# Performance work log

Measured on AMD Instinct MI355X. Metric: run time of the kernel, lower is better.

Reference implementation:

```python
import jax, jax.numpy as jnp
import numpy as np

A_NUM = 9
C_NUM = 20


def generate_anchor(anc, grid):
    # anc: (A,2) w,h ; grid: (B,H,W,2) centers -> anchors (B,A,H,W,4)
    centers = grid[:, None]                      # (B,1,H,W,2)
    half = anc.reshape(1, -1, 1, 1, 2) * 0.5     # (1,A,1,1,2)
    return jnp.concatenate([centers - half, centers + half], axis=-1)


def iou_matrix(proposals, bboxes):
    # proposals: (B,A,H,W,4) -> (B,K,4); bboxes: (B,N,5)
    B = proposals.shape[0]
    p = proposals.reshape(B, -1, 4)[:, :, None, :]   # (B,K,1,4)
    bb = bboxes[:, None, :, :]                       # (B,1,N,5)
    s_p = (p[..., 2] - p[..., 0]) * (p[..., 3] - p[..., 1])
    s_b = (bb[..., 2] - bb[..., 0]) * (bb[..., 3] - bb[..., 1])
    ix1 = jnp.maximum(p[..., 0], bb[..., 0])
    iy1 = jnp.maximum(p[..., 1], bb[..., 1])
    ix2 = jnp.minimum(p[..., 2], bb[..., 2])
    iy2 = jnp.minimum(p[..., 3], bb[..., 3])
    s_i = jnp.clip(ix2 - ix1, 0.0) * jnp.clip(iy2 - iy1, 0.0)
    s_u = s_p + s_b - s_i
    iou = jnp.clip(s_i / (s_u + 1e-8), 0.0)
    invalid = (s_u <= 0) | (s_p <= 0) | (s_b <= 0) | (bb[..., 0] < 0)
    return jnp.where(invalid, 0.0, iou)              # (B,K,N)


def extract_anchor_data(anchor_data, idx):
    # anchor_data: (B,A,D,H,W) -> flat (B*A*H*W, D) -> gather
    B, A, D, H, W = anchor_data.shape
    flat = jnp.transpose(anchor_data, (0, 1, 3, 4, 2)).reshape(-1, D)
    return flat[idx]


def extract_class_scores(all_scores, idx, num_anchors):
    # all_scores: (B,C,H,W) -> (B,A,H,W,C) flat -> gather
    B, C, H, W = all_scores.shape
    s = jnp.transpose(all_scores, (0, 2, 3, 1))[:, None]          # (B,1,H,W,C)
    s = jnp.broadcast_to(s, (B, num_anchors, H, W, C)).reshape(-1, C)
    return s[idx]


def setup_inputs() -> dict:
    key = jax.random.key(0)
    ks = jax.random.split(key, 8)
    B, Cin, H, W = 32, 1280, 28, 28
    N, M = 64, 4096
    hid, out_ch = 128, 5 * A_NUM + C_NUM
    features = jax.random.normal(ks[0], (B, Cin, H, W), dtype=jnp.float32)
    # grid of feature-cell centers (GenerateGrid-style)
    xs = jnp.arange(W, dtype=jnp.float32) + 0.5
    ys = jnp.arange(H, dtype=jnp.float32) + 0.5
    gx, gy = jnp.meshgrid(xs, ys, indexing='xy')
    grid = jnp.broadcast_to(jnp.stack([gx, gy], axis=-1), (B, H, W, 2))
    anc = jnp.array([[1.0, 1], [2, 2], [3, 3], [4, 4], [5, 5], [2, 3], [3, 2], [3, 5], [5, 3]], dtype=jnp.float32)
    tl = jax.random.uniform(ks[1], (B, N, 2), minval=0.0, maxval=20.0)
    wh = jax.random.uniform(ks[2], (B, N, 2), minval=1.0, maxval=8.0)
    cls = jax.random.randint(ks[3], (B, N, 1), 0, C_NUM).astype(jnp.float32)
    bb = jnp.concatenate([tl, tl + wh, cls], axis=-1)
    valid = jax.random.uniform(ks[4], (B, N, 1)) > 0.25
    bboxes = jnp.where(valid, bb, -1.0)
    K = B * A_NUM * H * W
    pos_anchor_idx = jax.random.randint(ks[5], (M,), 0, K, dtype=jnp.int64 if jax.config.jax_enable_x64 else jnp.int32)
    neg_anchor_idx = jax.random.randint(ks[6], (M,), 0, K, dtype=pos_anchor_idx.dtype)
    W1 = jax.random.normal(ks[7], (hid, Cin), dtype=jnp.float32) * 0.02
    b1 = jnp.zeros((hid,), dtype=jnp.float32)
    W2 = jax.random.normal(jax.random.fold_in(key, 99), (out_ch, hid), dtype=jnp.float32) * 0.02
    b2 = jnp.zeros((out_ch,), dtype=jnp.float32)
    return {"features": features, "grid": grid, "anc": anc, "bboxes": bboxes,
            "pos_anchor_idx": pos_anchor_idx, "neg_anchor_idx": neg_anchor_idx,
            "W1": W1, "b1": b1, "W2": W2, "b2": b2}


def reference(features, grid, anc, bboxes, pos_anchor_idx, neg_anchor_idx, W1, b1, W2, b2):
    B, Cin, H, W = features.shape
    A, C = A_NUM, C_NUM
    # anchors + broadcast IoU matrix
    anchors = generate_anchor(anc, grid)                 # (B,A,H,W,4)
    iou_mat = iou_matrix(anchors, bboxes)                # (B,A*H*W,N)
    # prediction head: 1x1 conv -> (dropout eval: identity) -> leaky_relu -> 1x1 conv
    h = jnp.einsum('bchw,oc->bohw', features, W1) + b1[None, :, None, None]
    h = jax.nn.leaky_relu(h, negative_slope=0.01)
    out = jnp.einsum('bchw,oc->bohw', h, W2) + b2[None, :, None, None]  # (B,5A+C,H,W)
    anchor_raw = out[:, :5 * A].reshape(B, A, 5, H, W)
    conf_sq = jax.nn.sigmoid(anchor_raw[:, :, 0:1])      # (B,A,1,H,W)
    off_raw = anchor_raw[:, :, 1:]                       # (B,A,4,H,W)
    off_sq = jnp.concatenate([jax.nn.sigmoid(off_raw[:, :, :2]) - 0.5, off_raw[:, :, 2:]], axis=2)
    class_raw = out[:, 5 * A:]                           # (B,C,H,W)
    # training path: irregular gathers
    class_scores = extract_class_scores(class_raw, pos_anchor_idx, A)   # (M,C)
    offsets = extract_anchor_data(off_sq, pos_anchor_idx)               # (M,4)
    conf_pos = extract_anchor_data(conf_sq, pos_anchor_idx)             # (M,1)
    conf_neg = extract_anchor_data(conf_sq, neg_anchor_idx)             # (M,1)
    conf_scores = jnp.concatenate([conf_pos, conf_neg], axis=0)         # (2M,1)
    return conf_scores, offsets, class_scores, iou_mat
```

## Files before the change

kernel.cpp:

```cpp
#include <hip/hip_runtime.h>
#include <cstdint>

#define A_NUM 9
#define C_NUM 20
#define B_SZ 32
#define HW 784
#define P_NUM (A_NUM*HW)
#define NBOX 64
#define CIN 1280
#define HID 128
#define M_IDX 4096
#define KS_W 10
#define HSTR2 136
#define OSTR 80
#define IOU_PB 64

#define CONF_OFF 0
#define OFFS_OFF (2*M_IDX)
#define CLS_OFF  (OFFS_OFF + 4*M_IDX)
#define IOU_OFF  (CLS_OFF + C_NUM*M_IDX)

#define GEMM_BLKS (B_SZ*49)
#define IOU_BX ((P_NUM + IOU_PB - 1)/IOU_PB)
#define IOU_BLKS (IOU_BX*B_SZ)

typedef short bf16x8 __attribute__((ext_vector_type(8)));
typedef float f32x4  __attribute__((ext_vector_type(4)));

__device__ __forceinline__ unsigned pack_bf16(float lo, float hi) {
  unsigned a = __builtin_bit_cast(unsigned, lo);
  unsigned b = __builtin_bit_cast(unsigned, hi);
  return ((a + 0x8000u) >> 16) | ((b + 0x8000u) & 0xffff0000u);
}

__global__ __launch_bounds__(256) void prep_w(const float* __restrict__ W1,
                                              const float* __restrict__ W2,
                                              uint4* __restrict__ W1f,
                                              uint4* __restrict__ W2f) {
  int id = blockIdx.x * 256 + threadIdx.x;
  if (id < 20480) {
    int lane = id & 63;
    int ntile = (id >> 6) & 7;
    int ks = id >> 9;
    int lo = lane & 15, quad = lane >> 4;
    int n = ntile * 16 + lo;
    int k0 = ks * 32 + quad * 8;
    const float* src = W1 + n * CIN + k0;
    float4 x = *(const float4*)src;
    float4 y = *(const float4*)(src + 4);
    uint4 p;
    p.x = pack_bf16(x.x, x.y);
    p.y = pack_bf16(x.z, x.w);
    p.z = pack_bf16(y.x, y.y);
    p.w = pack_bf16(y.z, y.w);
    W1f[id] = p;
  } else {
    int i2 = id - 20480;
    int lane = i2 & 63;
    int ntile = (i2 >> 6) % 5;
    int ks = i2 / 320;
    int lo = lane & 15, quad = lane >> 4;
    int n = ntile * 16 + lo;
    int k0 = ks * 32 + quad * 8;
    uint4 p = (uint4){0, 0, 0, 0};
    if (n < 5 * A_NUM + C_NUM) {
      const float* src = W2 + n * HID + k0;
      float4 x = *(const float4*)src;
      float4 y = *(const float4*)(src + 4);
      p.x = pack_bf16(x.x, x.y);
      p.y = pack_bf16(x.z, x.w);
      p.z = pack_bf16(y.x, y.y);
      p.w = pack_bf16(y.z, y.w);
    }
    W2f[i2] = p;
  }
}

union SharedU {
  struct {
    f32x4 red[4][8][64];
    unsigned short h[16 * HSTR2];
  } g;
  struct { float sb[NBOX * 5]; float4 sp4[IOU_PB]; } i;
};

__global__ __launch_bounds__(256) void fused_main(
    const float* __restrict__ F, const uint4* __restrict__ W1f,
    const uint4* __restrict__ W2f, const float* __restrict__ b1,
    const float* __restrict__ b2, float* __restrict__ Hd,
    const float* __restrict__ gridc, const float* __restrict__ anc,
    const float* __restrict__ bboxes, float* __restrict__ iou_out) {
  __shared__ SharedU sh;
  const int bid = blockIdx.x;
  const int t = threadIdx.x;

  if (bid >= GEMM_BLKS) {
    const int bid2 = bid - GEMM_BLKS;
    const int b = bid2 / IOU_BX;
    const int p0 = (bid2 - b * IOU_BX) * IOU_PB;
    float* sb = sh.i.sb;
    float4* sp4 = sh.i.sp4;
    for (int i = t; i < NBOX * 5; i += 256) sb[i] = bboxes[b * NBOX * 5 + i];
    if (t < IOU_PB) {
      int p = p0 + t;
      float x1 = 0.f, y1 = 0.f, x2 = 0.f, y2 = 0.f;
      if (p < P_NUM) {
        int a = p / HW, hw = p - a * HW;
        float2 c = ((const float2*)gridc)[b * HW + hw];
        float hx = anc[a * 2 + 0] * 0.5f, hy = anc[a * 2 + 1] * 0.5f;
        x1 = c.x - hx; y1 = c.y - hy; x2 = c.x + hx; y2 = c.y + hy;
      }
      sp4[t] = make_float4(x1, y1, x2, y2);
    }
    __syncthreads();
    const int nl = (t & 15) * 4;
    const int pi = t >> 4;
#pragma unroll
    for (int ip = 0; ip < 4; ip++) {
      const int pl = pi + 16 * ip;
      const int p = p0 + pl;
      const float4 pb = sp4[pl];
      const float spA = (pb.z - pb.x) * (pb.w - pb.y);
      float4 res;
#pragma unroll
      for (int jn = 0; jn < 4; jn++) {
        const int n = nl + jn;
        float bx1 = sb[n * 5 + 0], by1 = sb[n * 5 + 1];
        float bx2 = sb[n * 5 + 2], by2 = sb[n * 5 + 3];
        float s_b = (bx2 - bx1) * (by2 - by1);
        float ix1 = fmaxf(pb.x, bx1), iy1 = fmaxf(pb.y, by1);
        float ix2 = fminf(pb.z, bx2), iy2 = fminf(pb.w, by2);
        float si = fmaxf(ix2 - ix1, 0.f) * fmaxf(iy2 - iy1, 0.f);
        float su = spA + s_b - si;
        float iou = fmaxf(si / (su + 1e-8f), 0.f);
        bool invalid = (su <= 0.f) | (spA <= 0.f) | (s_b <= 0.f) | (bx1 < 0.f);
        float v = invalid ? 0.f : iou;
        if (jn == 0) res.x = v; else if (jn == 1) res.y = v;
        else if (jn == 2) res.z = v; else res.w = v;
      }
      if (p < P_NUM)
        *(float4*)&iou_out[((size_t)(b * P_NUM + p)) * 64 + nl] = res;
    }
    return;
  }

  const int w = t >> 6, lane = t & 63;
  const int quad = lane >> 4, lo = lane & 15;
  const int b = bid / 49;
  const int mf = bid - b * 49;
  const int m0 = mf * 16;

  const float* Fq = F + (size_t)b * CIN * HW +
                    (size_t)(w * (KS_W * 32) + quad * 8) * HW + m0 + lo;
  const uint4* Wq = W1f + (size_t)(w * KS_W) * 512 + lane;

  f32x4 acc[8];
#pragma unroll
  for (int i = 0; i < 8; i++) acc[i] = (f32x4){0.f, 0.f, 0.f, 0.f};

  float va0[8], va1[8];
  uint4 vb0[8], vb1[8];

  auto loadA = [&](int kk, float* va) {
    const float* p = Fq + (size_t)kk * 32 * HW;
#pragma unroll
    for (int j = 0; j < 8; j++) va[j] = p[(size_t)j * HW];
  };
  auto loadB = [&](int kk, uint4* vb) {
    const uint4* p = Wq + (size_t)kk * 512;
#pragma unroll
    for (int nf = 0; nf < 8; nf++) vb[nf] = p[nf * 64];
  };
  auto step = [&](const float* va, const uint4* vb) {
    uint4 ap;
    ap.x = pack_bf16(va[0], va[1]);
    ap.y = pack_bf16(va[2], va[3]);
    ap.z = pack_bf16(va[4], va[5]);
    ap.w = pack_bf16(va[6], va[7]);
    bf16x8 af = __builtin_bit_cast(bf16x8, ap);
#pragma unroll
    for (int nf = 0; nf < 8; nf++)
      acc[nf] = __builtin_amdgcn_mfma_f32_16x16x32_bf16(
          af, __builtin_bit_cast(bf16x8, vb[nf]), acc[nf], 0, 0, 0);
  };

  loadA(0, va0); loadB(0, vb0);
  loadA(1, va1); loadB(1, vb1);
#pragma unroll 2
  for (int kk = 0; kk < KS_W; kk += 2) {
    step(va0, vb0);
    if (kk + 2 < KS_W) { loadA(kk + 2, va0); loadB(kk + 2, vb0); }
    step(va1, vb1);
    if (kk + 3 < KS_W) { loadA(kk + 3, va1); loadB(kk + 3, vb1); }
  }

#pragma unroll
  for (int nf = 0; nf < 8; nf++) sh.g.red[w][nf][lane] = acc[nf];
  __syncthreads();

#pragma unroll
  for (int i = 0; i < 2; i++) {
    const int nf = 2 * w + i;
    f32x4 s = sh.g.red[0][nf][lane];
    s += sh.g.red[1][nf][lane];
    s += sh.g.red[2][nf][lane];
    s += sh.g.red[3][nf][lane];
    const float bb = b1[nf * 16 + lo];
#pragma unroll
    for (int r = 0; r < 4; r++) {
      float v = s[r] + bb;
      v = v > 0.f ? v : 0.01f * v;
      unsigned u = __builtin_bit_cast(unsigned, v);
      sh.g.h[(quad * 4 + r) * HSTR2 + nf * 16 + lo] =
          (unsigned short)((u + 0x8000u) >> 16);
    }
  }
  __syncthreads();

  {
    bf16x8 af[4];
#pragma unroll
    for (int ks = 0; ks < 4; ks++)
      af[ks] = *(const bf16x8*)(sh.g.h + lo * HSTR2 + ks * 32 + quad * 8);
    const int mrow = m0 + quad * 4;
#pragma unroll
    for (int rep = 0; rep < 2; rep++) {
      const int nt = rep ? 4 : w;
      if (rep && w != 0) break;
      f32x4 acc2 = (f32x4){0.f, 0.f, 0.f, 0.f};
#pragma unroll
      for (int ks = 0; ks < 4; ks++) {
        bf16x8 bf = __builtin_bit_cast(bf16x8, W2f[(ks * 5 + nt) * 64 + lane]);
        acc2 = __builtin_amdgcn_mfma_f32_16x16x32_bf16(af[ks], bf, acc2, 0, 0, 0);
      }
      const int o = nt * 16 + lo;
      if (o < 5 * A_NUM + C_NUM) {
        const float bz = b2[o];
        const int t5 = (o < 5 * A_NUM) ? (o % 5) : 5;
#pragma unroll
        for (int r = 0; r < 4; r++) {
          const int m = mrow + r;
          float v = acc2[r] + bz;
          if (t5 == 0) v = 1.f / (1.f + expf(-v));
          else if (t5 == 1 || t5 == 2) v = 1.f / (1.f + expf(-v)) - 0.5f;
          Hd[((size_t)b * HW + m) * OSTR + o] = v;
        }
      }
    }
  }
}

__global__ __launch_bounds__(256) void gather2(
    const int* __restrict__ pos_idx, const int* __restrict__ neg_idx,
    const float* __restrict__ Hd, float* __restrict__ out) {
  const int bid = blockIdx.x;
  if (bid < M_IDX / 8) {
    const int g = threadIdx.x >> 5;
    const int l = threadIdx.x & 31;
    const int slot = bid * 8 + g;
    const int idx = pos_idx[slot];
    const int b = idx / P_NUM, r = idx - b * P_NUM;
    const int a = r / HW, hw = r - a * HW;
    const float* row = Hd + ((size_t)b * HW + hw) * OSTR;
    if (l == 0)       out[CONF_OFF + slot] = row[a * 5];
    else if (l < 5)   out[OFFS_OFF + slot * 4 + (l - 1)] = row[a * 5 + l];
    else if (l < 25)  out[CLS_OFF + slot * C_NUM + (l - 5)] = row[5 * A_NUM + (l - 5)];
  } else {
    const int tt = (bid - M_IDX / 8) * 256 + threadIdx.x;
    if (tt < M_IDX) {
      const int idx = neg_idx[tt];
      const int b = idx / P_NUM, r = idx - b * P_NUM;
      const int a = r / HW, hw = r - a * HW;
      out[CONF_OFF + M_IDX + tt] = Hd[((size_t)b * HW + hw) * OSTR + a * 5];
    }
  }
}

extern "C" void kernel_launch(void* const* d_in, const int* in_sizes, int n_in,
                              void* d_out, int out_size, void* d_ws, size_t ws_size,
                              hipStream_t stream) {
  const float* features = (const float*)d_in[0];
  const float* gridc    = (const float*)d_in[1];
  const float* anc      = (const float*)d_in[2];
  const float* bboxes   = (const float*)d_in[3];
  const int*   pos_idx  = (const int*)d_in[4];
  const int*   neg_idx  = (const int*)d_in[5];
  const float* W1       = (const float*)d_in[6];
  const float* b1       = (const float*)d_in[7];
  const float* W2       = (const float*)d_in[8];
  const float* b2       = (const float*)d_in[9];
  float* out = (float*)d_out;

  uint4* W1f = (uint4*)d_ws;
  uint4* W2f = (uint4*)((char*)d_ws + 327680);
  float* Hd  = (float*)((char*)d_ws + 327680 + 20480);

  hipLaunchKernelGGL(prep_w, dim3(85), dim3(256), 0, stream, W1, W2, W1f, W2f);
  hipLaunchKernelGGL(fused_main, dim3(GEMM_BLKS + IOU_BLKS), dim3(256), 0, stream,
                     features, W1f, W2f, b1, b2, Hd,
                     gridc, anc, bboxes, out + IOU_OFF);
  hipLaunchKernelGGL(gather2, dim3(M_IDX / 8 + 16), dim3(256), 0, stream,
                     pos_idx, neg_idx, Hd, out);
}
```

Measured before the change: 255.8 us.

## Retile first GEMM to 32-row tiles with vectorized loads and LDS-staged A

The first 1x1-conv GEMM now uses 32-pixel M tiles split into two K halves and two N halves across the four waves. Feature rows are read as float4 vectors, converted to bf16, and staged through a swizzled, double-buffered LDS area instead of being gathered one scalar at a time per lane. The cross-wave reduction shrinks to adding two partial sums. IoU blocks are moved to the front of the grid. This targets uncoalesced feature loads and the redundant reloading of W1 for each 16-row tile, at the cost of more LDS traffic, more synchronisation, and clamped or masked handling of the partial last tile.

```diff
diff --git a/kernel.cpp b/kernel.cpp
--- a/kernel.cpp
+++ b/kernel.cpp
@@ -10,7 +10,7 @@
 #define CIN 1280
 #define HID 128
 #define M_IDX 4096
-#define KS_W 10
+#define KS_HALF 20
 #define HSTR2 136
 #define OSTR 80
 #define IOU_PB 64
@@ -20,9 +20,10 @@
 #define CLS_OFF  (OFFS_OFF + 4*M_IDX)
 #define IOU_OFF  (CLS_OFF + C_NUM*M_IDX)
 
-#define GEMM_BLKS (B_SZ*49)
 #define IOU_BX ((P_NUM + IOU_PB - 1)/IOU_PB)
 #define IOU_BLKS (IOU_BX*B_SZ)
+#define GEMM_MT 25
+#define GEMM_BLKS (GEMM_MT*B_SZ)
 
 typedef short bf16x8 __attribute__((ext_vector_type(8)));
 typedef float f32x4  __attribute__((ext_vector_type(4)));
@@ -78,8 +79,9 @@
 
 union SharedU {
   struct {
-    f32x4 red[4][8][64];
-    unsigned short h[16 * HSTR2];
+    unsigned short stage[4][2][1024];
+    f32x4 stash[2][2][4][64];
+    unsigned short h[32 * HSTR2];
   } g;
   struct { float sb[NBOX * 5]; float4 sp4[IOU_PB]; } i;
 };
@@ -94,10 +96,9 @@
   const int bid = blockIdx.x;
   const int t = threadIdx.x;
 
-  if (bid >= GEMM_BLKS) {
-    const int bid2 = bid - GEMM_BLKS;
-    const int b = bid2 / IOU_BX;
-    const int p0 = (bid2 - b * IOU_BX) * IOU_PB;
+  if (bid < IOU_BLKS) {
+    const int b = bid / IOU_BX;
+    const int p0 = (bid - b * IOU_BX) * IOU_PB;
     float* sb = sh.i.sb;
     float4* sp4 = sh.i.sp4;
     for (int i = t; i < NBOX * 5; i += 256) sb[i] = bboxes[b * NBOX * 5 + i];
@@ -144,102 +145,130 @@
     return;
   }
 
+  const int gid = bid - IOU_BLKS;
   const int w = t >> 6, lane = t & 63;
   const int quad = lane >> 4, lo = lane & 15;
-  const int b = bid / 49;
-  const int mf = bid - b * 49;
-  const int m0 = mf * 16;
-
-  const float* Fq = F + (size_t)b * CIN * HW +
-                    (size_t)(w * (KS_W * 32) + quad * 8) * HW + m0 + lo;
-  const uint4* Wq = W1f + (size_t)(w * KS_W) * 512 + lane;
-
-  f32x4 acc[8];
-#pragma unroll
-  for (int i = 0; i < 8; i++) acc[i] = (f32x4){0.f, 0.f, 0.f, 0.f};
-
-  float va0[8], va1[8];
-  uint4 vb0[8], vb1[8];
-
-  auto loadA = [&](int kk, float* va) {
-    const float* p = Fq + (size_t)kk * 32 * HW;
-#pragma unroll
-    for (int j = 0; j < 8; j++) va[j] = p[(size_t)j * HW];
+  const int ks = w >> 1, nh = w & 1;
+  const int b = gid / GEMM_MT;
+  const int mt = gid - b * GEMM_MT;
+  const int m0 = mt * 32;
+
+  const int kq = lane >> 3;
+  const int ml = (lane & 7) * 4;
+  const int mld = min(m0 + ml, HW - 4);
+  const float* Fb = F + (size_t)b * CIN * HW + mld + (size_t)(ks * 640 + kq * 4) * HW;
+  const int j0 = (kq & 1) * 4;
+
+  f32x4 acc[2][4];
+#pragma unroll
+  for (int i = 0; i < 2; i++)
+#pragma unroll
+    for (int j = 0; j < 4; j++) acc[i][j] = (f32x4){0.f, 0.f, 0.f, 0.f};
+
+  f32x4 ar0[4], ar1[4], ar2[4];
+  uint4 vb0[4], vb1[4];
+
+  auto loadA = [&](int kk, f32x4* ar) {
+    const float* p = Fb + (size_t)kk * 32 * HW;
+    ar[0] = *(const f32x4*)p;
+    ar[1] = *(const f32x4*)(p + HW);
+    ar[2] = *(const f32x4*)(p + 2 * HW);
+    ar[3] = *(const f32x4*)(p + 3 * HW);
   };
   auto loadB = [&](int kk, uint4* vb) {
-    const uint4* p = Wq + (size_t)kk * 512;
-#pragma unroll
-    for (int nf = 0; nf < 8; nf++) vb[nf] = p[nf * 64];
+    const uint4* p = W1f + ((size_t)(ks * KS_HALF + kk) * 8 + nh * 4) * 64 + lane;
+#pragma unroll
+    for (int nf = 0; nf < 4; nf++) vb[nf] = p[nf * 64];
   };
-  auto step = [&](const float* va, const uint4* vb) {
-    uint4 ap;
-    ap.x = pack_bf16(va[0], va[1]);
-    ap.y = pack_bf16(va[2], va[3]);
-    ap.z = pack_bf16(va[4], va[5]);
-    ap.w = pack_bf16(va[6], va[7]);
-    bf16x8 af = __builtin_bit_cast(bf16x8, ap);
-#pragma unroll
-    for (int nf = 0; nf < 8; nf++)
-      acc[nf] = __builtin_amdgcn_mfma_f32_16x16x32_bf16(
-          af, __builtin_bit_cast(bf16x8, vb[nf]), acc[nf], 0, 0, 0);
+  auto stageA = [&](int buf, f32x4* ar) {
+    char* sg = (char*)sh.g.stage[w][buf];
+#pragma unroll
+    for (int dm = 0; dm < 4; dm++) {
+      const int mloc = ml + dm;
+      const int mf = mloc >> 4;
+      const int lp = (lane >> 4) * 16 + (mloc & 15);
+      unsigned byte = mf * 1024 + lp * 16 + j0 * 2;
+      byte ^= ((unsigned)(lp >> 4) & 3u) << 5;
+      unsigned d0 = pack_bf16(ar[0][dm], ar[1][dm]);
+      unsigned d1 = pack_bf16(ar[2][dm], ar[3][dm]);
+      *(uint2*)(sg + byte) = (uint2){d0, d1};
+    }
   };
-
-  loadA(0, va0); loadB(0, vb0);
-  loadA(1, va1); loadB(1, vb1);
-#pragma unroll 2
-  for (int kk = 0; kk < KS_W; kk += 2) {
-    step(va0, vb0);
-    if (kk + 2 < KS_W) { loadA(kk + 2, va0); loadB(kk + 2, vb0); }
-    step(va1, vb1);
-    if (kk + 3 < KS_W) { loadA(kk + 3, va1); loadB(kk + 3, vb1); }
-  }
-
-#pragma unroll
-  for (int nf = 0; nf < 8; nf++) sh.g.red[w][nf][lane] = acc[nf];
+  auto compute = [&](int buf, uint4* vb) {
+    const char* sg = (const char*)sh.g.stage[w][buf];
+    bf16x8 af[2];
+#pragma unroll
+    for (int mf = 0; mf < 2; mf++) {
+      unsigned byte = mf * 1024 + lane * 16;
+      byte ^= ((unsigned)(lane >> 4) & 3u) << 5;
+      af[mf] = *(const bf16x8*)(sg + byte);
+    }
+#pragma unroll
+    for (int mf = 0; mf < 2; mf++)
+#pragma unroll
+      for (int nf = 0; nf < 4; nf++)
+        acc[mf][nf] = __builtin_amdgcn_mfma_f32_16x16x32_bf16(
+            af[mf], __builtin_bit_cast(bf16x8, vb[nf]), acc[mf][nf], 0, 0, 0);
+  };
+
+  loadA(0, ar0); loadA(1, ar1); loadA(2, ar2);
+  loadB(0, vb0); loadB(1, vb1);
+  stageA(0, ar0);
+#pragma unroll
+  for (int kk = 0; kk < KS_HALF; kk++) {
+    const int cur = kk & 1;
+    compute(cur, cur ? vb1 : vb0);
+    if (kk + 3 < KS_HALF) loadA(kk + 3, (kk % 3 == 0) ? ar0 : (kk % 3 == 1) ? ar1 : ar2);
+    if (kk + 2 < KS_HALF) loadB(kk + 2, cur ? vb1 : vb0);
+    if (kk + 1 < KS_HALF)
+      stageA(cur ^ 1, ((kk + 1) % 3 == 0) ? ar0 : ((kk + 1) % 3 == 1) ? ar1 : ar2);
+  }
+
+  if (ks == 1) {
+#pragma unroll
+    for (int mf = 0; mf < 2; mf++)
+#pragma unroll
+      for (int nf = 0; nf < 4; nf++) sh.g.stash[nh][mf][nf][lane] = acc[mf][nf];
+  }
   __syncthreads();
-
-#pragma unroll
-  for (int i = 0; i < 2; i++) {
-    const int nf = 2 * w + i;
-    f32x4 s = sh.g.red[0][nf][lane];
-    s += sh.g.red[1][nf][lane];
-    s += sh.g.red[2][nf][lane];
-    s += sh.g.red[3][nf][lane];
-    const float bb = b1[nf * 16 + lo];
-#pragma unroll
-    for (int r = 0; r < 4; r++) {
-      float v = s[r] + bb;
-      v = v > 0.f ? v : 0.01f * v;
-      unsigned u = __builtin_bit_cast(unsigned, v);
-      sh.g.h[(quad * 4 + r) * HSTR2 + nf * 16 + lo] =
-          (unsigned short)((u + 0x8000u) >> 16);
+  if (ks == 0) {
+#pragma unroll
+    for (int mf = 0; mf < 2; mf++) {
+#pragma unroll
+      for (int nf = 0; nf < 4; nf++) {
+        f32x4 s = acc[mf][nf] + sh.g.stash[nh][mf][nf][lane];
+        const float bb = b1[nh * 64 + nf * 16 + lo];
+#pragma unroll
+        for (int r = 0; r < 4; r++) {
+          float v = s[r] + bb;
+          v = v > 0.f ? v : 0.01f * v;
+          unsigned u = __builtin_bit_cast(unsigned, v);
+          sh.g.h[(mf * 16 + quad * 4 + r) * HSTR2 + nh * 64 + nf * 16 + lo] =
+              (unsigned short)((u + 0x8000u) >> 16);
+        }
+      }
     }
   }
   __syncthreads();
 
-  {
-    bf16x8 af[4];
-#pragma unroll
-    for (int ks = 0; ks < 4; ks++)
-      af[ks] = *(const bf16x8*)(sh.g.h + lo * HSTR2 + ks * 32 + quad * 8);
-    const int mrow = m0 + quad * 4;
-#pragma unroll
-    for (int rep = 0; rep < 2; rep++) {
-      const int nt = rep ? 4 : w;
-      if (rep && w != 0) break;
-      f32x4 acc2 = (f32x4){0.f, 0.f, 0.f, 0.f};
-#pragma unroll
-      for (int ks = 0; ks < 4; ks++) {
-        bf16x8 bf = __builtin_bit_cast(bf16x8, W2f[(ks * 5 + nt) * 64 + lane]);
-        acc2 = __builtin_amdgcn_mfma_f32_16x16x32_bf16(af[ks], bf, acc2, 0, 0, 0);
-      }
-      const int o = nt * 16 + lo;
-      if (o < 5 * A_NUM + C_NUM) {
-        const float bz = b2[o];
-        const int t5 = (o < 5 * A_NUM) ? (o % 5) : 5;
-#pragma unroll
-        for (int r = 0; r < 4; r++) {
-          const int m = mrow + r;
+  for (int id = w; id < 10; id += 4) {
+    const int mf = id / 5, nt = id - (id / 5) * 5;
+    f32x4 acc2 = (f32x4){0.f, 0.f, 0.f, 0.f};
+#pragma unroll
+    for (int k2 = 0; k2 < 4; k2++) {
+      bf16x8 haf = *(const bf16x8*)&sh.g.h[(mf * 16 + lo) * HSTR2 + k2 * 32 + quad * 8];
+      bf16x8 bf = __builtin_bit_cast(bf16x8, W2f[(k2 * 5 + nt) * 64 + lane]);
+      acc2 = __builtin_amdgcn_mfma_f32_16x16x32_bf16(haf, bf, acc2, 0, 0, 0);
+    }
+    const int o = nt * 16 + lo;
+    if (o < 5 * A_NUM + C_NUM) {
+      const float bz = b2[o];
+      const int t5 = (o < 5 * A_NUM) ? (o % 5) : 5;
+      const int mrow = m0 + mf * 16 + quad * 4;
+#pragma unroll
+      for (int r = 0; r < 4; r++) {
+        const int m = mrow + r;
+        if (m < HW) {
           float v = acc2[r] + bz;
           if (t5 == 0) v = 1.f / (1.f + expf(-v));
           else if (t5 == 1 || t5 == 2) v = 1.f / (1.f + expf(-v)) - 0.5f;
@@ -296,7 +325,7 @@
   float* Hd  = (float*)((char*)d_ws + 327680 + 20480);
 
   hipLaunchKernelGGL(prep_w, dim3(85), dim3(256), 0, stream, W1, W2, W1f, W2f);
-  hipLaunchKernelGGL(fused_main, dim3(GEMM_BLKS + IOU_BLKS), dim3(256), 0, stream,
+  hipLaunchKernelGGL(fused_main, dim3(IOU_BLKS + GEMM_BLKS), dim3(256), 0, stream,
                      features, W1f, W2f, b1, b2, Hd,
                      gridc, anc, bboxes, out + IOU_OFF);
   hipLaunchKernelGGL(gather2, dim3(M_IDX / 8 + 16), dim3(256), 0, stream,
```

Result: no change. 260.7 us (+1.9%).

## Restructure GEMM to 32-row tiles with LDS-staged, double-buffered feature loads

Applied to the files above, without the earlier changes.

The first 1x1-conv GEMM now gives each block a 32-pixel tile and the full K range. Waves split the N dimension instead of K, which removes the cross-wave reduction through shared memory. Feature data is loaded coalesced as float4, transposed into a double-buffered LDS tile and read back as MFMA fragments, with a three-deep register prefetch. The costs are a __syncthreads per K step, fewer blocks (25 instead of 49 per batch), and clamped or masked edge handling because 784 is not a multiple of 32.

```diff
diff --git a/kernel.cpp b/kernel.cpp
--- a/kernel.cpp
+++ b/kernel.cpp
@@ -10,7 +10,8 @@
 #define CIN 1280
 #define HID 128
 #define M_IDX 4096
-#define KS_W 10
+#define KS_ALL 40
+#define ASTR3 36
 #define HSTR2 136
 #define OSTR 80
 #define IOU_PB 64
@@ -20,7 +21,8 @@
 #define CLS_OFF  (OFFS_OFF + 4*M_IDX)
 #define IOU_OFF  (CLS_OFF + C_NUM*M_IDX)
 
-#define GEMM_BLKS (B_SZ*49)
+#define GEMM_MT 25
+#define GEMM_BLKS (GEMM_MT*B_SZ)
 #define IOU_BX ((P_NUM + IOU_PB - 1)/IOU_PB)
 #define IOU_BLKS (IOU_BX*B_SZ)
 
@@ -78,8 +80,8 @@
 
 union SharedU {
   struct {
-    f32x4 red[4][8][64];
-    unsigned short h[16 * HSTR2];
+    float As[2][32 * ASTR3];
+    unsigned short h[32 * HSTR2];
   } g;
   struct { float sb[NBOX * 5]; float4 sp4[IOU_PB]; } i;
 };
@@ -146,100 +148,107 @@
 
   const int w = t >> 6, lane = t & 63;
   const int quad = lane >> 4, lo = lane & 15;
-  const int b = bid / 49;
-  const int mf = bid - b * 49;
-  const int m0 = mf * 16;
-
-  const float* Fq = F + (size_t)b * CIN * HW +
-                    (size_t)(w * (KS_W * 32) + quad * 8) * HW + m0 + lo;
-  const uint4* Wq = W1f + (size_t)(w * KS_W) * 512 + lane;
-
-  f32x4 acc[8];
-#pragma unroll
-  for (int i = 0; i < 8; i++) acc[i] = (f32x4){0.f, 0.f, 0.f, 0.f};
-
-  float va0[8], va1[8];
-  uint4 vb0[8], vb1[8];
-
-  auto loadA = [&](int kk, float* va) {
-    const float* p = Fq + (size_t)kk * 32 * HW;
-#pragma unroll
-    for (int j = 0; j < 8; j++) va[j] = p[(size_t)j * HW];
+  const int b = bid / GEMM_MT;
+  const int mt = bid - b * GEMM_MT;
+  const int m0 = mt * 32;
+
+  const int cl = t >> 3;
+  const int mq = t & 7;
+  const int mld = min(m0 + 4 * mq, HW - 4);
+  const float* Fb = F + ((size_t)b * CIN + cl) * HW + mld;
+
+  f32x4 acc[2][2];
+#pragma unroll
+  for (int i = 0; i < 2; i++)
+#pragma unroll
+    for (int j = 0; j < 2; j++) acc[i][j] = (f32x4){0.f, 0.f, 0.f, 0.f};
+
+  float4 rg[3];
+  uint4 vb[3][2];
+
+  auto loadF = [&](int kk, float4* r) {
+    *r = *(const float4*)(Fb + (size_t)kk * 32 * HW);
   };
-  auto loadB = [&](int kk, uint4* vb) {
-    const uint4* p = Wq + (size_t)kk * 512;
-#pragma unroll
-    for (int nf = 0; nf < 8; nf++) vb[nf] = p[nf * 64];
+  auto loadB = [&](int kk, uint4* v) {
+    const uint4* p = W1f + (size_t)kk * 512 + 2 * w * 64 + lane;
+    v[0] = p[0];
+    v[1] = p[64];
   };
-  auto step = [&](const float* va, const uint4* vb) {
-    uint4 ap;
-    ap.x = pack_bf16(va[0], va[1]);
-    ap.y = pack_bf16(va[2], va[3]);
-    ap.z = pack_bf16(va[4], va[5]);
-    ap.w = pack_bf16(va[6], va[7]);
-    bf16x8 af = __builtin_bit_cast(bf16x8, ap);
-#pragma unroll
-    for (int nf = 0; nf < 8; nf++)
-      acc[nf] = __builtin_amdgcn_mfma_f32_16x16x32_bf16(
-          af, __builtin_bit_cast(bf16x8, vb[nf]), acc[nf], 0, 0, 0);
+  auto stage = [&](int buf, const float4& r) {
+    float* d = &sh.g.As[buf][(4 * mq) * ASTR3 + cl];
+    d[0] = r.x; d[ASTR3] = r.y; d[2 * ASTR3] = r.z; d[3 * ASTR3] = r.w;
   };
-
-  loadA(0, va0); loadB(0, vb0);
-  loadA(1, va1); loadB(1, vb1);
-#pragma unroll 2
-  for (int kk = 0; kk < KS_W; kk += 2) {
-    step(va0, vb0);
-    if (kk + 2 < KS_W) { loadA(kk + 2, va0); loadB(kk + 2, vb0); }
-    step(va1, vb1);
-    if (kk + 3 < KS_W) { loadA(kk + 3, va1); loadB(kk + 3, vb1); }
-  }
-
-#pragma unroll
-  for (int nf = 0; nf < 8; nf++) sh.g.red[w][nf][lane] = acc[nf];
+  auto compute = [&](int buf, uint4* v) {
+    const float* Ab = &sh.g.As[buf][lo * ASTR3 + quad * 8];
+#pragma unroll
+    for (int i = 0; i < 2; i++) {
+      f32x4 a0 = *(const f32x4*)(Ab + i * 16 * ASTR3);
+      f32x4 a1 = *(const f32x4*)(Ab + i * 16 * ASTR3 + 4);
+      uint4 ap;
+      ap.x = pack_bf16(a0[0], a0[1]);
+      ap.y = pack_bf16(a0[2], a0[3]);
+      ap.z = pack_bf16(a1[0], a1[1]);
+      ap.w = pack_bf16(a1[2], a1[3]);
+      bf16x8 af = __builtin_bit_cast(bf16x8, ap);
+#pragma unroll
+      for (int nf = 0; nf < 2; nf++)
+        acc[i][nf] = __builtin_amdgcn_mfma_f32_16x16x32_bf16(
+            af, __builtin_bit_cast(bf16x8, v[nf]), acc[i][nf], 0, 0, 0);
+    }
+  };
+
+  loadF(0, &rg[0]); loadF(1, &rg[1]);
+  loadB(0, vb[0]); loadB(1, vb[1]);
+  stage(0, rg[0]);
   __syncthreads();
+#pragma unroll
+  for (int kk = 0; kk < KS_ALL; kk++) {
+    const int cur = kk & 1;
+    if (kk + 2 < KS_ALL) {
+      loadF(kk + 2, &rg[(kk + 2) % 3]);
+      loadB(kk + 2, vb[(kk + 2) % 3]);
+    }
+    compute(cur, vb[kk % 3]);
+    if (kk + 1 < KS_ALL) stage(cur ^ 1, rg[(kk + 1) % 3]);
+    __syncthreads();
+  }
 
 #pragma unroll
   for (int i = 0; i < 2; i++) {
-    const int nf = 2 * w + i;
-    f32x4 s = sh.g.red[0][nf][lane];
-    s += sh.g.red[1][nf][lane];
-    s += sh.g.red[2][nf][lane];
-    s += sh.g.red[3][nf][lane];
-    const float bb = b1[nf * 16 + lo];
-#pragma unroll
-    for (int r = 0; r < 4; r++) {
-      float v = s[r] + bb;
-      v = v > 0.f ? v : 0.01f * v;
-      unsigned u = __builtin_bit_cast(unsigned, v);
-      sh.g.h[(quad * 4 + r) * HSTR2 + nf * 16 + lo] =
-          (unsigned short)((u + 0x8000u) >> 16);
+#pragma unroll
+    for (int nf = 0; nf < 2; nf++) {
+      const int n = w * 32 + nf * 16 + lo;
+      const float bb = b1[n];
+#pragma unroll
+      for (int r = 0; r < 4; r++) {
+        float v = acc[i][nf][r] + bb;
+        v = v > 0.f ? v : 0.01f * v;
+        unsigned u = __builtin_bit_cast(unsigned, v);
+        sh.g.h[(i * 16 + quad * 4 + r) * HSTR2 + n] =
+            (unsigned short)((u + 0x8000u) >> 16);
+      }
     }
   }
   __syncthreads();
 
-  {
-    bf16x8 af[4];
-#pragma unroll
-    for (int ks = 0; ks < 4; ks++)
-      af[ks] = *(const bf16x8*)(sh.g.h + lo * HSTR2 + ks * 32 + quad * 8);
-    const int mrow = m0 + quad * 4;
-#pragma unroll
-    for (int rep = 0; rep < 2; rep++) {
-      const int nt = rep ? 4 : w;
-      if (rep && w != 0) break;
-      f32x4 acc2 = (f32x4){0.f, 0.f, 0.f, 0.f};
-#pragma unroll
-      for (int ks = 0; ks < 4; ks++) {
-        bf16x8 bf = __builtin_bit_cast(bf16x8, W2f[(ks * 5 + nt) * 64 + lane]);
-        acc2 = __builtin_amdgcn_mfma_f32_16x16x32_bf16(af[ks], bf, acc2, 0, 0, 0);
-      }
-      const int o = nt * 16 + lo;
-      if (o < 5 * A_NUM + C_NUM) {
-        const float bz = b2[o];
-        const int t5 = (o < 5 * A_NUM) ? (o % 5) : 5;
-#pragma unroll
-        for (int r = 0; r < 4; r++) {
-          const int m = mrow + r;
+  for (int id = w; id < 10; id += 4) {
+    const int mf = id / 5, nt = id - (id / 5) * 5;
+    f32x4 acc2 = (f32x4){0.f, 0.f, 0.f, 0.f};
+#pragma unroll
+    for (int k2 = 0; k2 < 4; k2++) {
+      bf16x8 haf = *(const bf16x8*)&sh.g.h[(mf * 16 + lo) * HSTR2 + k2 * 32 + quad * 8];
+      bf16x8 bf = __builtin_bit_cast(bf16x8, W2f[(k2 * 5 + nt) * 64 + lane]);
+      acc2 = __builtin_amdgcn_mfma_f32_16x16x32_bf16(haf, bf, acc2, 0, 0, 0);
+    }
+    const int o = nt * 16 + lo;
+    if (o < 5 * A_NUM + C_NUM) {
+      const float bz = b2[o];
+      const int t5 = (o < 5 * A_NUM) ? (o % 5) : 5;
+      const int mrow = m0 + mf * 16 + quad * 4;
+#pragma unroll
+      for (int r = 0; r < 4; r++) {
+        const int m = mrow + r;
+        if (m < HW) {
           float v = acc2[r] + bz;
           if (t5 == 0) v = 1.f / (1.f + expf(-v));
           else if (t5 == 1 || t5 == 2) v = 1.f / (1.f + expf(-v)) - 0.5f;
```

Result: faster. 243.4 us (-4.9%).

## Split feature transpose to bf16 from GEMM and use single-wave full-K GEMM

Applied to the files above, without the earlier changes.

Adds a pass that transposes the fp32 features into a K-contiguous bf16 MFMA fragment layout in workspace, fused with the IOU blocks. The head GEMM then runs as one-wave blocks over the full K, with no cross-wave shared-memory reduction. This removes strided fp32 loads and the in-loop bf16 packing from the GEMM. In exchange it writes and rereads an extra 64 MB intermediate and adds a kernel launch.

```diff
diff --git a/kernel.cpp b/kernel.cpp
--- a/kernel.cpp
+++ b/kernel.cpp
@@ -10,7 +10,7 @@
 #define CIN 1280
 #define HID 128
 #define M_IDX 4096
-#define KS_W 10
+#define KS_ALL 40
 #define HSTR2 136
 #define OSTR 80
 #define IOU_PB 64
@@ -20,9 +20,10 @@
 #define CLS_OFF  (OFFS_OFF + 4*M_IDX)
 #define IOU_OFF  (CLS_OFF + C_NUM*M_IDX)
 
-#define GEMM_BLKS (B_SZ*49)
+#define TRANS_BLKS (B_SZ*KS_ALL)
 #define IOU_BX ((P_NUM + IOU_PB - 1)/IOU_PB)
 #define IOU_BLKS (IOU_BX*B_SZ)
+#define GEMM_WAVES (B_SZ*49)
 
 typedef short bf16x8 __attribute__((ext_vector_type(8)));
 typedef float f32x4  __attribute__((ext_vector_type(4)));
@@ -76,175 +77,175 @@
   }
 }
 
-union SharedU {
-  struct {
-    f32x4 red[4][8][64];
-    unsigned short h[16 * HSTR2];
-  } g;
+union SharedT {
+  struct { float tile[32][136]; } t;
   struct { float sb[NBOX * 5]; float4 sp4[IOU_PB]; } i;
 };
 
-__global__ __launch_bounds__(256) void fused_main(
-    const float* __restrict__ F, const uint4* __restrict__ W1f,
-    const uint4* __restrict__ W2f, const float* __restrict__ b1,
-    const float* __restrict__ b2, float* __restrict__ Hd,
+__global__ __launch_bounds__(256) void trans_iou(
+    const float* __restrict__ F, uint4* __restrict__ Af,
     const float* __restrict__ gridc, const float* __restrict__ anc,
     const float* __restrict__ bboxes, float* __restrict__ iou_out) {
-  __shared__ SharedU sh;
+  __shared__ SharedT sh;
   const int bid = blockIdx.x;
   const int t = threadIdx.x;
 
-  if (bid >= GEMM_BLKS) {
-    const int bid2 = bid - GEMM_BLKS;
-    const int b = bid2 / IOU_BX;
-    const int p0 = (bid2 - b * IOU_BX) * IOU_PB;
-    float* sb = sh.i.sb;
-    float4* sp4 = sh.i.sp4;
-    for (int i = t; i < NBOX * 5; i += 256) sb[i] = bboxes[b * NBOX * 5 + i];
-    if (t < IOU_PB) {
-      int p = p0 + t;
-      float x1 = 0.f, y1 = 0.f, x2 = 0.f, y2 = 0.f;
-      if (p < P_NUM) {
-        int a = p / HW, hw = p - a * HW;
-        float2 c = ((const float2*)gridc)[b * HW + hw];
-        float hx = anc[a * 2 + 0] * 0.5f, hy = anc[a * 2 + 1] * 0.5f;
-        x1 = c.x - hx; y1 = c.y - hy; x2 = c.x + hx; y2 = c.y + hy;
+  if (bid < TRANS_BLKS) {
+    const int b = bid / KS_ALL, ks = bid - b * KS_ALL;
+    const float* Fsrc = F + ((size_t)b * CIN + ks * 32) * HW;
+    uint4* Adst = Af + (size_t)(b * KS_ALL + ks) * (HW * 4);
+    const int row = t >> 3, s0 = t & 7;
+    const int tm = t >> 1, hh = t & 1;
+    for (int ch = 0; ch < 7; ch++) {
+      const int mbase = ch * 128;
+      const int W = (ch < 6) ? 128 : 16;
+#pragma unroll
+      for (int i = 0; i < 4; i++) {
+        const int slot = s0 + 8 * i;
+        if (slot * 4 < W) {
+          float4 v = *(const float4*)(Fsrc + (size_t)row * HW + mbase + slot * 4);
+          *(float4*)&sh.t.tile[row][slot * 4] = v;
+        }
       }
-      sp4[t] = make_float4(x1, y1, x2, y2);
-    }
-    __syncthreads();
-    const int nl = (t & 15) * 4;
-    const int pi = t >> 4;
-#pragma unroll
-    for (int ip = 0; ip < 4; ip++) {
-      const int pl = pi + 16 * ip;
-      const int p = p0 + pl;
-      const float4 pb = sp4[pl];
-      const float spA = (pb.z - pb.x) * (pb.w - pb.y);
-      float4 res;
-#pragma unroll
-      for (int jn = 0; jn < 4; jn++) {
-        const int n = nl + jn;
-        float bx1 = sb[n * 5 + 0], by1 = sb[n * 5 + 1];
-        float bx2 = sb[n * 5 + 2], by2 = sb[n * 5 + 3];
-        float s_b = (bx2 - bx1) * (by2 - by1);
-        float ix1 = fmaxf(pb.x, bx1), iy1 = fmaxf(pb.y, by1);
-        float ix2 = fminf(pb.z, bx2), iy2 = fminf(pb.w, by2);
-        float si = fmaxf(ix2 - ix1, 0.f) * fmaxf(iy2 - iy1, 0.f);
-        float su = spA + s_b - si;
-        float iou = fmaxf(si / (su + 1e-8f), 0.f);
-        bool invalid = (su <= 0.f) | (spA <= 0.f) | (s_b <= 0.f) | (bx1 < 0.f);
-        float v = invalid ? 0.f : iou;
-        if (jn == 0) res.x = v; else if (jn == 1) res.y = v;
-        else if (jn == 2) res.z = v; else res.w = v;
+      __syncthreads();
+      if (tm < W) {
+        const int m = mbase + tm;
+        unsigned d[8];
+#pragma unroll
+        for (int j = 0; j < 8; j++)
+          d[j] = pack_bf16(sh.t.tile[16 * hh + 2 * j][tm],
+                           sh.t.tile[16 * hh + 2 * j + 1][tm]);
+        Adst[m * 4 + 2 * hh]     = (uint4){d[0], d[1], d[2], d[3]};
+        Adst[m * 4 + 2 * hh + 1] = (uint4){d[4], d[5], d[6], d[7]};
       }
-      if (p < P_NUM)
-        *(float4*)&iou_out[((size_t)(b * P_NUM + p)) * 64 + nl] = res;
+      __syncthreads();
     }
     return;
   }
 
-  const int w = t >> 6, lane = t & 63;
-  const int quad = lane >> 4, lo = lane & 15;
-  const int b = bid / 49;
-  const int mf = bid - b * 49;
+  const int bid2 = bid - TRANS_BLKS;
+  const int b = bid2 / IOU_BX;
+  const int p0 = (bid2 - b * IOU_BX) * IOU_PB;
+  float* sb = sh.i.sb;
+  float4* sp4 = sh.i.sp4;
+  for (int i = t; i < NBOX * 5; i += 256) sb[i] = bboxes[b * NBOX * 5 + i];
+  if (t < IOU_PB) {
+    int p = p0 + t;
+    float x1 = 0.f, y1 = 0.f, x2 = 0.f, y2 = 0.f;
+    if (p < P_NUM) {
+      int a = p / HW, hw = p - a * HW;
+      float2 c = ((const float2*)gridc)[b * HW + hw];
+      float hx = anc[a * 2 + 0] * 0.5f, hy = anc[a * 2 + 1] * 0.5f;
+      x1 = c.x - hx; y1 = c.y - hy; x2 = c.x + hx; y2 = c.y + hy;
+    }
+    sp4[t] = make_float4(x1, y1, x2, y2);
+  }
+  __syncthreads();
+  const int nl = (t & 15) * 4;
+  const int pi = t >> 4;
+#pragma unroll
+  for (int ip = 0; ip < 4; ip++) {
+    const int pl = pi + 16 * ip;
+    const int p = p0 + pl;
+    const float4 pb = sp4[pl];
+    const float spA = (pb.z - pb.x) * (pb.w - pb.y);
+    float4 res;
+#pragma unroll
+    for (int jn = 0; jn < 4; jn++) {
+      const int n = nl + jn;
+      float bx1 = sb[n * 5 + 0], by1 = sb[n * 5 + 1];
+      float bx2 = sb[n * 5 + 2], by2 = sb[n * 5 + 3];
+      float s_b = (bx2 - bx1) * (by2 - by1);
+      float ix1 = fmaxf(pb.x, bx1), iy1 = fmaxf(pb.y, by1);
+      float ix2 = fminf(pb.z, bx2), iy2 = fminf(pb.w, by2);
+      float si = fmaxf(ix2 - ix1, 0.f) * fmaxf(iy2 - iy1, 0.f);
+      float su = spA + s_b - si;
+      float iou = fmaxf(si / (su + 1e-8f), 0.f);
+      bool invalid = (su <= 0.f) | (spA <= 0.f) | (s_b <= 0.f) | (bx1 < 0.f);
+      float v = invalid ? 0.f : iou;
+      if (jn == 0) res.x = v; else if (jn == 1) res.y = v;
+      else if (jn == 2) res.z = v; else res.w = v;
+    }
+    if (p < P_NUM)
+      *(float4*)&iou_out[((size_t)(b * P_NUM + p)) * 64 + nl] = res;
+  }
+}
+
+__global__ __launch_bounds__(64) void gemm_head(
+    const uint4* __restrict__ Af, const uint4* __restrict__ W1f,
+    const uint4* __restrict__ W2f, const float* __restrict__ b1,
+    const float* __restrict__ b2, float* __restrict__ Hd) {
+  __shared__ unsigned short h[16 * HSTR2];
+  const int g = blockIdx.x;
+  const int b = g / 49, mf = g - b * 49;
   const int m0 = mf * 16;
-
-  const float* Fq = F + (size_t)b * CIN * HW +
-                    (size_t)(w * (KS_W * 32) + quad * 8) * HW + m0 + lo;
-  const uint4* Wq = W1f + (size_t)(w * KS_W) * 512 + lane;
+  const int lane = threadIdx.x & 63, quad = lane >> 4, lo = lane & 15;
+
+  const uint4* Aw = Af + (size_t)(b * KS_ALL) * (HW * 4) + (m0 + lo) * 4 + quad;
+  const uint4* Bw = W1f + lane;
 
   f32x4 acc[8];
 #pragma unroll
   for (int i = 0; i < 8; i++) acc[i] = (f32x4){0.f, 0.f, 0.f, 0.f};
 
-  float va0[8], va1[8];
-  uint4 vb0[8], vb1[8];
-
-  auto loadA = [&](int kk, float* va) {
-    const float* p = Fq + (size_t)kk * 32 * HW;
-#pragma unroll
-    for (int j = 0; j < 8; j++) va[j] = p[(size_t)j * HW];
+  uint4 a[4];
+  uint4 vb[2][8];
+
+  auto loadB = [&](int s, uint4* dst) {
+#pragma unroll
+    for (int nt = 0; nt < 8; nt++) dst[nt] = Bw[(size_t)(s * 8 + nt) * 64];
   };
-  auto loadB = [&](int kk, uint4* vb) {
-    const uint4* p = Wq + (size_t)kk * 512;
-#pragma unroll
-    for (int nf = 0; nf < 8; nf++) vb[nf] = p[nf * 64];
-  };
-  auto step = [&](const float* va, const uint4* vb) {
-    uint4 ap;
-    ap.x = pack_bf16(va[0], va[1]);
-    ap.y = pack_bf16(va[2], va[3]);
-    ap.z = pack_bf16(va[4], va[5]);
-    ap.w = pack_bf16(va[6], va[7]);
-    bf16x8 af = __builtin_bit_cast(bf16x8, ap);
-#pragma unroll
-    for (int nf = 0; nf < 8; nf++)
-      acc[nf] = __builtin_amdgcn_mfma_f32_16x16x32_bf16(
-          af, __builtin_bit_cast(bf16x8, vb[nf]), acc[nf], 0, 0, 0);
-  };
-
-  loadA(0, va0); loadB(0, vb0);
-  loadA(1, va1); loadB(1, vb1);
-#pragma unroll 2
-  for (int kk = 0; kk < KS_W; kk += 2) {
-    step(va0, vb0);
-    if (kk + 2 < KS_W) { loadA(kk + 2, va0); loadB(kk + 2, vb0); }
-    step(va1, vb1);
-    if (kk + 3 < KS_W) { loadA(kk + 3, va1); loadB(kk + 3, vb1); }
-  }
-
-#pragma unroll
-  for (int nf = 0; nf < 8; nf++) sh.g.red[w][nf][lane] = acc[nf];
-  __syncthreads();
-
-#pragma unroll
-  for (int i = 0; i < 2; i++) {
-    const int nf = 2 * w + i;
-    f32x4 s = sh.g.red[0][nf][lane];
-    s += sh.g.red[1][nf][lane];
-    s += sh.g.red[2][nf][lane];
-    s += sh.g.red[3][nf][lane];
-    const float bb = b1[nf * 16 + lo];
+
+  loadB(0, vb[0]);
+#pragma unroll
+  for (int i = 0; i < 4; i++) a[i] = Aw[(size_t)i * (HW * 4)];
+
+#pragma unroll
+  for (int s = 0; s < KS_ALL; s++) {
+    bf16x8 av = __builtin_bit_cast(bf16x8, a[s & 3]);
+    if (s + 1 < KS_ALL) loadB(s + 1, vb[(s + 1) & 1]);
+    if (s + 4 < KS_ALL) a[(s + 4) & 3] = Aw[(size_t)(s + 4) * (HW * 4)];
+#pragma unroll
+    for (int nt = 0; nt < 8; nt++)
+      acc[nt] = __builtin_amdgcn_mfma_f32_16x16x32_bf16(
+          av, __builtin_bit_cast(bf16x8, vb[s & 1][nt]), acc[nt], 0, 0, 0);
+  }
+
+#pragma unroll
+  for (int nt = 0; nt < 8; nt++) {
+    const float bb = b1[nt * 16 + lo];
 #pragma unroll
     for (int r = 0; r < 4; r++) {
-      float v = s[r] + bb;
+      float v = acc[nt][r] + bb;
       v = v > 0.f ? v : 0.01f * v;
       unsigned u = __builtin_bit_cast(unsigned, v);
-      sh.g.h[(quad * 4 + r) * HSTR2 + nf * 16 + lo] =
+      h[(quad * 4 + r) * HSTR2 + nt * 16 + lo] =
           (unsigned short)((u + 0x8000u) >> 16);
     }
   }
   __syncthreads();
 
-  {
-    bf16x8 af[4];
-#pragma unroll
-    for (int ks = 0; ks < 4; ks++)
-      af[ks] = *(const bf16x8*)(sh.g.h + lo * HSTR2 + ks * 32 + quad * 8);
-    const int mrow = m0 + quad * 4;
-#pragma unroll
-    for (int rep = 0; rep < 2; rep++) {
-      const int nt = rep ? 4 : w;
-      if (rep && w != 0) break;
-      f32x4 acc2 = (f32x4){0.f, 0.f, 0.f, 0.f};
-#pragma unroll
-      for (int ks = 0; ks < 4; ks++) {
-        bf16x8 bf = __builtin_bit_cast(bf16x8, W2f[(ks * 5 + nt) * 64 + lane]);
-        acc2 = __builtin_amdgcn_mfma_f32_16x16x32_bf16(af[ks], bf, acc2, 0, 0, 0);
-      }
-      const int o = nt * 16 + lo;
-      if (o < 5 * A_NUM + C_NUM) {
-        const float bz = b2[o];
-        const int t5 = (o < 5 * A_NUM) ? (o % 5) : 5;
-#pragma unroll
-        for (int r = 0; r < 4; r++) {
-          const int m = mrow + r;
-          float v = acc2[r] + bz;
-          if (t5 == 0) v = 1.f / (1.f + expf(-v));
-          else if (t5 == 1 || t5 == 2) v = 1.f / (1.f + expf(-v)) - 0.5f;
-          Hd[((size_t)b * HW + m) * OSTR + o] = v;
-        }
+#pragma unroll
+  for (int nt = 0; nt < 5; nt++) {
+    f32x4 a2 = (f32x4){0.f, 0.f, 0.f, 0.f};
+#pragma unroll
+    for (int k2 = 0; k2 < 4; k2++) {
+      bf16x8 haf = *(const bf16x8*)&h[lo * HSTR2 + k2 * 32 + quad * 8];
+      bf16x8 bf = __builtin_bit_cast(bf16x8, W2f[(k2 * 5 + nt) * 64 + lane]);
+      a2 = __builtin_amdgcn_mfma_f32_16x16x32_bf16(haf, bf, a2, 0, 0, 0);
+    }
+    const int o = nt * 16 + lo;
+    if (o < 5 * A_NUM + C_NUM) {
+      const float bz = b2[o];
+      const int t5 = (o < 5 * A_NUM) ? (o % 5) : 5;
+      const int mrow = m0 + quad * 4;
+#pragma unroll
+      for (int r = 0; r < 4; r++) {
+        const int m = mrow + r;
+        float v = a2[r] + bz;
+        if (t5 == 0) v = 1.f / (1.f + expf(-v));
+        else if (t5 == 1 || t5 == 2) v = 1.f / (1.f + expf(-v)) - 0.5f;
+        Hd[((size_t)b * HW + m) * OSTR + o] = v;
       }
     }
   }
@@ -293,12 +294,14 @@
 
   uint4* W1f = (uint4*)d_ws;
   uint4* W2f = (uint4*)((char*)d_ws + 327680);
-  float* Hd  = (float*)((char*)d_ws + 327680 + 20480);
+  uint4* Af  = (uint4*)((char*)d_ws + 348160);
+  float* Hd  = (float*)((char*)d_ws + 348160 + 64225280);
 
   hipLaunchKernelGGL(prep_w, dim3(85), dim3(256), 0, stream, W1, W2, W1f, W2f);
-  hipLaunchKernelGGL(fused_main, dim3(GEMM_BLKS + IOU_BLKS), dim3(256), 0, stream,
-                     features, W1f, W2f, b1, b2, Hd,
-                     gridc, anc, bboxes, out + IOU_OFF);
+  hipLaunchKernelGGL(trans_iou, dim3(TRANS_BLKS + IOU_BLKS), dim3(256), 0, stream,
+                     features, Af, gridc, anc, bboxes, out + IOU_OFF);
+  hipLaunchKernelGGL(gemm_head, dim3(GEMM_WAVES), dim3(64), 0, stream,
+                     Af, W1f, W2f, b1, b2, Hd);
   hipLaunchKernelGGL(gather2, dim3(M_IDX / 8 + 16), dim3(256), 0, stream,
                      pos_idx, neg_idx, Hd, out);
 }
```

After: 271.5 us. 6.1% more time.
